# Performance work log

Hardware: AMD Instinct MI355X
Metric: run time of the kernel (lower is better)

## Reference

```python
import jax, jax.numpy as jnp
import numpy as np

TWN_THRESHOLD_FACTOR = 0.05
BN_EPS = 1e-5


def ternary_quantize(w):
    # threshold = 0.05 * max|w| (detached); q in {-1, 0, +1}
    t = TWN_THRESHOLD_FACTOR * jnp.max(jnp.abs(jax.lax.stop_gradient(w)))
    return (w > t).astype(w.dtype) - (w < -t).astype(w.dtype)


def conv2d(x, w, b):
    q = ternary_quantize(w)
    y = jax.lax.conv_general_dilated(x, q, (1, 1), 'VALID',
                                     dimension_numbers=('NCHW', 'OIHW', 'NCHW'))
    return y + b[None, :, None, None]


def linear(x, w, b):
    q = ternary_quantize(w)
    return x @ q.T + b


def bn_train(x, gamma, beta, axes):
    # training-mode batch norm (biased variance), matches torch BN in train()
    mean = jnp.mean(x, axis=axes, keepdims=True)
    var = jnp.var(x, axis=axes, keepdims=True)
    xhat = (x - mean) * jax.lax.rsqrt(var + BN_EPS)
    shape = [1] * x.ndim
    shape[1] = x.shape[1]
    return xhat * gamma.reshape(shape) + beta.reshape(shape)


def maxpool2(x):
    return jax.lax.reduce_window(x, -jnp.inf, jax.lax.max,
                                 (1, 1, 2, 2), (1, 1, 2, 2), 'VALID')


def setup_inputs() -> dict:
    key = jax.random.key(0)
    ks = jax.random.split(key, 8)
    B, Cin, H, W = 512, 1, 28, 28
    C1, C2, K = 64, 128, 5
    FLAT, F1, F2 = 4 * 4 * C2, 512, 10
    inp = {
        'x': jax.random.normal(ks[0], (B, Cin, H, W), jnp.float32),
        'conv1_w': jax.random.normal(ks[1], (C1, Cin, K, K), jnp.float32) * (1.0 / np.sqrt(Cin * K * K)),
        'conv1_b': jax.random.normal(ks[2], (C1,), jnp.float32) * 0.05,
        'bn1_g': jnp.ones((C1,), jnp.float32),
        'bn1_b': jnp.zeros((C1,), jnp.float32),
        'conv2_w': jax.random.normal(ks[3], (C2, C1, K, K), jnp.float32) * (1.0 / np.sqrt(C1 * K * K)),
        'conv2_b': jax.random.normal(ks[4], (C2,), jnp.float32) * 0.05,
        'bn2_g': jnp.ones((C2,), jnp.float32),
        'bn2_b': jnp.zeros((C2,), jnp.float32),
        'fc1_w': jax.random.normal(ks[5], (F1, FLAT), jnp.float32) * (1.0 / np.sqrt(FLAT)),
        'fc1_b': jax.random.normal(ks[6], (F1,), jnp.float32) * 0.05,
        'bn3_g': jnp.ones((F1,), jnp.float32),
        'bn3_b': jnp.zeros((F1,), jnp.float32),
        'fc2_w': jax.random.normal(ks[7], (F2, F1), jnp.float32) * (1.0 / np.sqrt(F1)),
        'fc2_b': jnp.zeros((F2,), jnp.float32),
    }
    return inp


def reference(x, conv1_w, conv1_b, bn1_g, bn1_b, conv2_w, conv2_b, bn2_g, bn2_b,
              fc1_w, fc1_b, bn3_g, bn3_b, fc2_w, fc2_b):
    h = jax.nn.relu(bn_train(conv2d(x, conv1_w, conv1_b), bn1_g, bn1_b, (0, 2, 3)))
    h = maxpool2(h)  # [B, 64, 12, 12]
    h = jax.nn.relu(bn_train(conv2d(h, conv2_w, conv2_b), bn2_g, bn2_b, (0, 2, 3)))
    h = maxpool2(h)  # [B, 128, 4, 4]
    h = h.reshape(h.shape[0], -1)  # [B, 2048]
    h = jax.nn.relu(bn_train(linear(h, fc1_w, fc1_b), bn3_g, bn3_b, (0,)))
    return linear(h, fc2_w, fc2_b)  # [B, 10]
```

## Files before the change

kernel.cpp:

```cpp
#include <hip/hip_runtime.h>
#include <stdint.h>

#define EPS 1e-5f

typedef short v8s __attribute__((ext_vector_type(8)));
typedef float v4f __attribute__((ext_vector_type(4)));

static const size_t W1F   = 4096;
static const size_t W2F   = 8192;
static const size_t WF2F  = 212992;
static const size_t A_F   = 262144;
static const size_t PMN2F = 4980736;
static const size_t B_F   = 19136512;
static const size_t WF1T  = B_F + 1048576;

__device__ inline unsigned short f2bf(float f) {
    unsigned u = __float_as_uint(f);
    return (unsigned short)((u + 0x7FFF + ((u >> 16) & 1)) >> 16);
}

__device__ __forceinline__ void stage16(const unsigned short* g, unsigned short* l) {
    __builtin_amdgcn_global_load_lds(
        (const __attribute__((address_space(1))) unsigned int*)g,
        (__attribute__((address_space(3))) unsigned int*)l, 16, 0, 0);
}

__global__ void k_zero(float* p, int n) {
    int i = blockIdx.x * blockDim.x + threadIdx.x;
    if (i < n) p[i] = 0.f;
}

__global__ void k_absmax4(const float* __restrict__ w0, int n0,
                          const float* __restrict__ w1, int n1,
                          const float* __restrict__ w2, int n2,
                          const float* __restrict__ w3, int n3,
                          float* outv) {
    int blk = blockIdx.x;
    const float* w; int n; unsigned* out; int nb; int bi;
    if (blk < 1)        { w = w0; n = n0; out = (unsigned*)(outv + 0); nb = 1;   bi = blk;      }
    else if (blk < 17)  { w = w1; n = n1; out = (unsigned*)(outv + 1); nb = 16;  bi = blk - 1;  }
    else if (blk < 209) { w = w2; n = n2; out = (unsigned*)(outv + 2); nb = 192; bi = blk - 17; }
    else                { w = w3; n = n3; out = (unsigned*)(outv + 3); nb = 1;   bi = blk - 209; }
    float m = 0.f;
    for (int i = bi * 256 + threadIdx.x; i < n; i += nb * 256)
        m = fmaxf(m, fabsf(w[i]));
    #pragma unroll
    for (int o = 32; o; o >>= 1) m = fmaxf(m, __shfl_down(m, o));
    if ((threadIdx.x & 63) == 0) atomicMax(out, __float_as_uint(m));
}

__global__ void k_quantE(const float* __restrict__ c1w, const float* __restrict__ c2w,
                         const float* __restrict__ f2w, const float* __restrict__ am,
                         float* __restrict__ w1t, unsigned short* __restrict__ w2u,
                         float* __restrict__ wf2) {
    int blk = blockIdx.x;
    if (blk < 1) {
        float t = 0.05f * am[0];
        for (int i = threadIdx.x; i < 1600; i += 256) {
            float v = c1w[i];
            float q = (float)((v > t) - (v < -t));
            int c = i / 25, k = i - c * 25;
            w1t[k * 64 + c] = q;
        }
    } else if (blk < 401) {
        float t = 0.05f * am[1];
        int base = (blk - 1) * 512;
        #pragma unroll
        for (int jj = 0; jj < 2; ++jj) {
            int i = base + jj * 256 + threadIdx.x;
            int j    = i & 7;
            int lane = (i >> 3) & 63;
            int mt   = (i >> 9) & 7;
            int ks   = (i >> 12) & 1;
            int p    = i >> 13;
            int c  = mt * 16 + (lane & 15);
            int ci = ks * 32 + (lane >> 4) * 8 + j;
            float v = c2w[c * 1600 + ci * 25 + p];
            w2u[i] = (v > t) ? (unsigned short)0x3F80
                             : ((v < -t) ? (unsigned short)0xBF80 : (unsigned short)0);
        }
    } else {
        float t = 0.05f * am[3];
        for (int i = threadIdx.x; i < 5120; i += 256) {
            float v = f2w[i];
            wf2[i] = (float)((v > t) - (v < -t));
        }
    }
}

__global__ __launch_bounds__(512) void k_conv1(const float* __restrict__ x,
                                               const float* __restrict__ w1t,
                                               unsigned* __restrict__ pmn1,
                                               float* __restrict__ sum,
                                               float* __restrict__ ssq) {
    __shared__ float xs[784];
    __shared__ float red[2][8][64];
    int b = blockIdx.x;
    const float4* xim = (const float4*)(x + (size_t)b * 784);
    for (int i = threadIdx.x; i < 196; i += 512) ((float4*)xs)[i] = xim[i];
    int c  = threadIdx.x & 63;
    int wv = threadIdx.x >> 6;
    float w[25];
    #pragma unroll
    for (int k = 0; k < 25; ++k) w[k] = w1t[k * 64 + c];
    __syncthreads();
    unsigned* ob = pmn1 + (size_t)b * 9216;
    float s = 0.f, s2 = 0.f;
    int ph = 0, pw = wv;
    for (int it = 0; it < 18; ++it) {
        const float* xp = xs + (ph * 2) * 28 + pw * 2;
        float win[36];
        #pragma unroll
        for (int i = 0; i < 6; ++i)
            #pragma unroll
            for (int j = 0; j < 3; ++j) {
                float2 t2 = *(const float2*)(xp + i * 28 + j * 2);
                win[i * 6 + j * 2] = t2.x; win[i * 6 + j * 2 + 1] = t2.y;
            }
        float v00 = 0.f, v01 = 0.f, v10 = 0.f, v11 = 0.f;
        #pragma unroll
        for (int i = 0; i < 5; ++i)
            #pragma unroll
            for (int j = 0; j < 5; ++j) {
                float wk = w[i * 5 + j];
                v00 = fmaf(win[i * 6 + j],           wk, v00);
                v01 = fmaf(win[i * 6 + j + 1],       wk, v01);
                v10 = fmaf(win[(i + 1) * 6 + j],     wk, v10);
                v11 = fmaf(win[(i + 1) * 6 + j + 1], wk, v11);
            }
        s  += v00 + v01 + v10 + v11;
        s2 += v00 * v00 + v01 * v01 + v10 * v10 + v11 * v11;
        float mx = fmaxf(fmaxf(v00, v01), fmaxf(v10, v11));
        float mn = fminf(fminf(v00, v01), fminf(v10, v11));
        ob[(ph * 12 + pw) * 64 + c] = ((unsigned)f2bf(mx) << 16) | (unsigned)f2bf(mn);
        pw += 8; if (pw >= 12) { pw -= 12; ++ph; }
    }
    red[0][wv][c] = s; red[1][wv][c] = s2;
    __syncthreads();
    if (threadIdx.x < 64) {
        float S = 0.f, S2 = 0.f;
        #pragma unroll
        for (int i = 0; i < 8; ++i) { S += red[0][i][threadIdx.x]; S2 += red[1][i][threadIdx.x]; }
        atomicAdd(&sum[threadIdx.x], S);
        atomicAdd(&ssq[threadIdx.x], S2);
    }
}

__global__ __launch_bounds__(256) void k_conv2(const unsigned* __restrict__ pmn1,
                                               const unsigned short* __restrict__ wfrag,
                                               const float* __restrict__ c1sum,
                                               const float* __restrict__ c1ssq,
                                               const float* __restrict__ g1,
                                               const float* __restrict__ b1,
                                               float* __restrict__ pmn,
                                               float* __restrict__ sum,
                                               float* __restrict__ ssq) {
    __shared__ unsigned short xs[144 * 76];
    __shared__ unsigned short wb[2][4096];
    __shared__ float reds[2][64], redq[2][64];
    int b     = blockIdx.x >> 1;
    int mhalf = blockIdx.x & 1;
    int tid  = threadIdx.x;
    int lane = tid & 63;
    int wave = tid >> 6;
    int nh = wave & 1, kp = wave >> 1;

    int ch0 = (tid & 15) * 4;
    float scv[4], shv[4];
    {
        const float invN = 1.f / 294912.f;
        #pragma unroll
        for (int j = 0; j < 4; ++j) {
            int ch = ch0 + j;
            float mean = c1sum[ch] * invN;
            float var  = c1ssq[ch] * invN - mean * mean;
            scv[j] = g1[ch] * rsqrtf(var + EPS);
            shv[j] = b1[ch] - mean * scv[j];
        }
    }
    const uint4* srcp = (const uint4*)(pmn1 + (size_t)b * 9216);
    for (int it = 0; it < 9; ++it) {
        int i = it * 256 + tid;
        int r = i >> 4;
        uint4 u4 = srcp[i];
        unsigned long long pack = 0;
        #pragma unroll
        for (int j = 0; j < 4; ++j) {
            unsigned u = (&u4.x)[j];
            float mx = __uint_as_float(u & 0xffff0000u);
            float mn = __uint_as_float(u << 16);
            float v = (scv[j] > 0.f) ? mx : mn;
            unsigned short o = f2bf(fmaxf(0.f, fmaf(v, scv[j], shv[j])));
            pack |= ((unsigned long long)o) << (16 * j);
        }
        *(unsigned long long*)(&xs[r * 76 + ch0]) = pack;
    }
    #pragma unroll
    for (int h = 0; h < 2; ++h) {
        int ksm = wave * 2 + h;
        int ks = ksm >> 2, mt = ksm & 3;
        const unsigned short* g = wfrag + (size_t)(ks * 8 + mhalf * 4 + mt) * 512 + lane * 8;
        stage16(g, &wb[0][ks * 2048 + mt * 512 + lane * 8]);
    }
    __syncthreads();

    int n = lane & 15, quad = lane >> 4;
    int ow = n & 7;
    int ohb0 = nh * 4 + (n >> 3);
    int col0 = kp * 32 + quad * 8;
    v4f acc[4][2];
    #pragma unroll
    for (int mm = 0; mm < 4; ++mm) { acc[mm][0] = (v4f){0,0,0,0}; acc[mm][1] = (v4f){0,0,0,0}; }
    for (int p = 0; p < 25; ++p) {
        int cur = p & 1;
        if (p < 24) {
            #pragma unroll
            for (int h = 0; h < 2; ++h) {
                int ksm = wave * 2 + h;
                int ks = ksm >> 2, mt = ksm & 3;
                const unsigned short* g = wfrag +
                    (size_t)(((p + 1) * 2 + ks) * 8 + mhalf * 4 + mt) * 512 + lane * 8;
                stage16(g, &wb[cur ^ 1][ks * 2048 + mt * 512 + lane * 8]);
            }
        }
        int kh = p / 5, kw = p - (p / 5) * 5;
        int col = (ow + kw) * 76 + col0;
        v8s bf0 = *(const v8s*)(&xs[(ohb0 + kh) * 912 + col]);
        v8s bf1 = *(const v8s*)(&xs[(ohb0 + 2 + kh) * 912 + col]);
        #pragma unroll
        for (int mm = 0; mm < 4; ++mm) {
            v8s af = *(const v8s*)(&wb[cur][kp * 2048 + mm * 512 + lane * 8]);
            acc[mm][0] = __builtin_amdgcn_mfma_f32_16x16x32_bf16(af, bf0, acc[mm][0], 0, 0, 0);
            acc[mm][1] = __builtin_amdgcn_mfma_f32_16x16x32_bf16(af, bf1, acc[mm][1], 0, 0, 0);
        }
        __syncthreads();
    }
    float* mbuf = (float*)xs;
    if (kp == 1) {
        float* d = mbuf + (nh * 64 + lane) * 36;
        #pragma unroll
        for (int mm = 0; mm < 4; ++mm) {
            *(v4f*)(d + mm * 8)     = acc[mm][0];
            *(v4f*)(d + mm * 8 + 4) = acc[mm][1];
        }
    }
    __syncthreads();
    if (kp == 0) {
        const float* s = mbuf + (nh * 64 + lane) * 36;
        #pragma unroll
        for (int mm = 0; mm < 4; ++mm) {
            acc[mm][0] += *(const v4f*)(s + mm * 8);
            acc[mm][1] += *(const v4f*)(s + mm * 8 + 4);
        }
        float* po = pmn + (size_t)b * 4096;
        #pragma unroll
        for (int mm = 0; mm < 4; ++mm) {
            int cl0 = mm * 16 + quad * 4;
            #pragma unroll
            for (int r = 0; r < 4; ++r) {
                int cl = cl0 + r;
                int c  = mhalf * 64 + cl;
                float sA = 0.f, s2A = 0.f;
                #pragma unroll
                for (int bf = 0; bf < 2; ++bf) {
                    float v = acc[mm][bf][r];
                    float pm = fmaxf(v, __shfl_xor(v, 1));
                    float pn = fminf(v, __shfl_xor(v, 1));
                    pm = fmaxf(pm, __shfl_xor(pm, 8));
                    pn = fminf(pn, __shfl_xor(pn, 8));
                    if (((n & 1) == 0) && (n < 8)) {
                        int psp = (nh * 2 + bf) * 4 + (n >> 1);
                        *(float2*)(&po[(c * 16 + psp) * 2]) = make_float2(pm, pn);
                    }
                    float s = v, s2 = v * v;
                    #pragma unroll
                    for (int m = 1; m < 16; m <<= 1) { s += __shfl_xor(s, m); s2 += __shfl_xor(s2, m); }
                    sA += s; s2A += s2;
                }
                if (n == 0) { reds[nh][cl] = sA; redq[nh][cl] = s2A; }
            }
        }
    }
    __syncthreads();
    if (tid < 64) {
        atomicAdd(&sum[mhalf * 64 + tid], reds[0][tid] + reds[1][tid]);
        atomicAdd(&ssq[mhalf * 64 + tid], redq[0][tid] + redq[1][tid]);
    }
}

__global__ void k_prep_fc1(const float* __restrict__ w, const float* __restrict__ am,
                           unsigned short* __restrict__ wf,
                           const float* __restrict__ pmn2, const float* __restrict__ c2sum,
                           const float* __restrict__ c2ssq, const float* __restrict__ g2,
                           const float* __restrict__ b2, unsigned short* __restrict__ xfrag) {
    if (blockIdx.x < 4096) {
        float t = 0.05f * am[2];
        int i = blockIdx.x * 256 + threadIdx.x;
        int f = i >> 11, k = i & 2047;
        float v = w[i];
        unsigned short q = (v > t) ? (unsigned short)0x3F80
                         : ((v < -t) ? (unsigned short)0xBF80 : (unsigned short)0);
        int ft = f >> 4, fm = f & 15;
        int ks = k >> 5, kr = k & 31;
        int lane = (kr >> 3) * 16 + fm;
        wf[((size_t)(ks * 32 + ft) * 64 + lane) * 8 + (kr & 7)] = q;
    } else {
        int i = (blockIdx.x - 4096) * 256 + threadIdx.x;
        int j    = i & 7;
        int lane = (i >> 3) & 63;
        int bt   = (i >> 9) & 31;
        int ks   = i >> 14;
        int b = bt * 16 + (lane & 15);
        int k = ks * 32 + (lane >> 4) * 8 + j;
        int c = k >> 4, psp = k & 15;
        float2 mm = *(const float2*)(&pmn2[((size_t)b * 2048 + c * 16 + psp) * 2]);
        float mean = c2sum[c] * (1.f / 32768.f);
        float var  = c2ssq[c] * (1.f / 32768.f) - mean * mean;
        float sc = g2[c] * rsqrtf(var + EPS);
        float sh = b2[c] - mean * sc;
        float v = (sc > 0.f) ? mm.x : mm.y;
        xfrag[i] = f2bf(fmaxf(0.f, fmaf(v, sc, sh)));
    }
}

__global__ __launch_bounds__(256) void k_fc1(const unsigned short* __restrict__ xfrag,
                                             const unsigned short* __restrict__ wfrag,
                                             float* __restrict__ out,
                                             float* __restrict__ sum,
                                             float* __restrict__ ssq) {
    int lane = threadIdx.x & 63;
    int wave = threadIdx.x >> 6;
    int ft = (blockIdx.x & 7) * 4 + wave;
    int bT = blockIdx.x >> 3;
    v4f acc = (v4f){0.f, 0.f, 0.f, 0.f};
    for (int ks = 0; ks < 64; ++ks) {
        v8s bfrag = *(const v8s*)(xfrag + ((size_t)(ks * 32 + bT) * 64 + lane) * 8);
        v8s afrag = *(const v8s*)(wfrag + ((size_t)(ks * 32 + ft) * 64 + lane) * 8);
        acc = __builtin_amdgcn_mfma_f32_16x16x32_bf16(afrag, bfrag, acc, 0, 0, 0);
    }
    int bb = bT * 16 + (lane & 15);
    int quad = lane >> 4;
    int f0 = ft * 16 + quad * 4;
    *(float4*)(&out[(size_t)bb * 512 + f0]) =
        make_float4(acc[0], acc[1], acc[2], acc[3]);
    #pragma unroll
    for (int r = 0; r < 4; ++r) {
        float s = acc[r], s2 = s * s;
        #pragma unroll
        for (int m = 1; m < 16; m <<= 1) { s += __shfl_xor(s, m); s2 += __shfl_xor(s2, m); }
        if ((lane & 15) == 0) { atomicAdd(&sum[f0 + r], s); atomicAdd(&ssq[f0 + r], s2); }
    }
}

__global__ __launch_bounds__(256) void k_fc2(const float* __restrict__ x,
                                             const float* __restrict__ w,
                                             const float* __restrict__ bias,
                                             const float* __restrict__ fsum,
                                             const float* __restrict__ fssq,
                                             const float* __restrict__ g3,
                                             const float* __restrict__ b3,
                                             float* __restrict__ out) {
    int lane = threadIdx.x & 63;
    int b = blockIdx.x * 4 + (threadIdx.x >> 6);
    float xa[8], sm[8], sq[8], ga[8], ba[8];
    {
        const float4* p;
        p = (const float4*)(x + (size_t)b * 512 + lane * 8);
        *(float4*)xa = p[0]; *(float4*)(xa + 4) = p[1];
        p = (const float4*)(fsum + lane * 8);
        *(float4*)sm = p[0]; *(float4*)(sm + 4) = p[1];
        p = (const float4*)(fssq + lane * 8);
        *(float4*)sq = p[0]; *(float4*)(sq + 4) = p[1];
        p = (const float4*)(g3 + lane * 8);
        *(float4*)ga = p[0]; *(float4*)(ga + 4) = p[1];
        p = (const float4*)(b3 + lane * 8);
        *(float4*)ba = p[0]; *(float4*)(ba + 4) = p[1];
    }
    float h[8];
    #pragma unroll
    for (int e = 0; e < 8; ++e) {
        float mean = sm[e] * (1.f / 512.f);
        float var  = sq[e] * (1.f / 512.f) - mean * mean;
        float sc = ga[e] * rsqrtf(var + EPS);
        float sh = ba[e] - mean * sc;
        h[e] = fmaxf(0.f, fmaf(xa[e], sc, sh));
    }
    #pragma unroll
    for (int j = 0; j < 10; ++j) {
        const float4* wp = (const float4*)(w + j * 512 + lane * 8);
        float4 w0 = wp[0], w1 = wp[1];
        float p = h[0] * w0.x + h[1] * w0.y + h[2] * w0.z + h[3] * w0.w
                + h[4] * w1.x + h[5] * w1.y + h[6] * w1.z + h[7] * w1.w;
        #pragma unroll
        for (int o = 32; o; o >>= 1) p += __shfl_down(p, o);
        if (lane == 0) out[b * 10 + j] = p + bias[j];
    }
}

extern "C" void kernel_launch(void* const* d_in, const int* in_sizes, int n_in,
                              void* d_out, int out_size, void* d_ws, size_t ws_size,
                              hipStream_t stream) {
    const float* x       = (const float*)d_in[0];
    const float* conv1_w = (const float*)d_in[1];
    const float* bn1_g   = (const float*)d_in[3];
    const float* bn1_b   = (const float*)d_in[4];
    const float* conv2_w = (const float*)d_in[5];
    const float* bn2_g   = (const float*)d_in[7];
    const float* bn2_b   = (const float*)d_in[8];
    const float* fc1_w   = (const float*)d_in[9];
    const float* bn3_g   = (const float*)d_in[11];
    const float* bn3_b   = (const float*)d_in[12];
    const float* fc2_w   = (const float*)d_in[13];
    const float* fc2_b   = (const float*)d_in[14];

    float* wsf = (float*)d_ws;

    float* c1_sum = wsf + 16,   * c1_ssq = wsf + 80;
    float* c2_sum = wsf + 272,  * c2_ssq = wsf + 400;
    float* f_sum  = wsf + 1808, * f_ssq  = wsf + 2320;

    float* w1t = wsf + W1F;
    unsigned short* w2u = (unsigned short*)(wsf + W2F);
    float* wf2 = wsf + WF2F;
    unsigned short* wf1 = (unsigned short*)(wsf + WF1T);
    unsigned* PMN1 = (unsigned*)(wsf + A_F);
    float* PMN2 = wsf + PMN2F;
    float* A    = wsf + A_F;
    unsigned short* xfrag = (unsigned short*)(wsf + B_F);

    k_zero<<<16, 256, 0, stream>>>(wsf, 4096);

    k_absmax4<<<210, 256, 0, stream>>>(conv1_w, 1600, conv2_w, 204800,
                                       fc1_w, 1048576, fc2_w, 5120, wsf);

    k_quantE<<<402, 256, 0, stream>>>(conv1_w, conv2_w, fc2_w, wsf, w1t, w2u, wf2);

    k_conv1<<<512, 512, 0, stream>>>(x, w1t, PMN1, c1_sum, c1_ssq);

    k_conv2<<<1024, 256, 0, stream>>>(PMN1, w2u, c1_sum, c1_ssq, bn1_g, bn1_b,
                                      PMN2, c2_sum, c2_ssq);

    k_prep_fc1<<<8192, 256, 0, stream>>>(fc1_w, wsf, wf1, PMN2, c2_sum, c2_ssq,
                                         bn2_g, bn2_b, xfrag);

    k_fc1<<<256, 256, 0, stream>>>(xfrag, wf1, A, f_sum, f_ssq);

    k_fc2<<<128, 256, 0, stream>>>(A, wf2, fc2_b, f_sum, f_ssq, bn3_g, bn3_b,
                                   (float*)d_out);
}
```

Baseline: 201.3 us.

## Fuse zeroing, absmax and weight quantization into fewer launches; streamline conv2 loop

Merges the zero, absmax and quantize kernels into two launches. Absmax now writes per-block partial maxima instead of using atomics, and conv1 quantizes its own weights inline. fc1 weight quantization moves into the conv1 launch as extra blocks, so it runs concurrently instead of in a later prep kernel. The conv2 main loop is restructured with a lambda that uses incremental pointers and ping-pong buffers to remove per-iteration index arithmetic. Every consumer block re-reduces up to 192 partial maxima serially, which adds some redundant work.

Measured after the change: 210.7 us. +4.7%, slower.

```diff
diff --git a/kernel.cpp b/kernel.cpp
--- a/kernel.cpp
+++ b/kernel.cpp
@@ -6,7 +6,6 @@
 typedef short v8s __attribute__((ext_vector_type(8)));
 typedef float v4f __attribute__((ext_vector_type(4)));
 
-static const size_t W1F   = 4096;
 static const size_t W2F   = 8192;
 static const size_t WF2F  = 212992;
 static const size_t A_F   = 262144;
@@ -14,6 +13,11 @@
 static const size_t B_F   = 19136512;
 static const size_t WF1T  = B_F + 1048576;
 
+#define P_C1 1024
+#define P_F2 1025
+#define P_C2 1040
+#define P_F1 1240
+
 __device__ inline unsigned short f2bf(float f) {
     unsigned u = __float_as_uint(f);
     return (unsigned short)((u + 0x7FFF + ((u >> 16) & 1)) >> 16);
@@ -25,84 +29,106 @@
         (__attribute__((address_space(3))) unsigned int*)l, 16, 0, 0);
 }
 
-__global__ void k_zero(float* p, int n) {
-    int i = blockIdx.x * blockDim.x + threadIdx.x;
-    if (i < n) p[i] = 0.f;
-}
-
-__global__ void k_absmax4(const float* __restrict__ w0, int n0,
-                          const float* __restrict__ w1, int n1,
-                          const float* __restrict__ w2, int n2,
-                          const float* __restrict__ w3, int n3,
-                          float* outv) {
+__global__ void k_absz(const float* __restrict__ c1w, const float* __restrict__ c2w,
+                       const float* __restrict__ f1w, const float* __restrict__ f2w,
+                       float* __restrict__ wsf) {
+    __shared__ float sm4[4];
     int blk = blockIdx.x;
-    const float* w; int n; unsigned* out; int nb; int bi;
-    if (blk < 1)        { w = w0; n = n0; out = (unsigned*)(outv + 0); nb = 1;   bi = blk;      }
-    else if (blk < 17)  { w = w1; n = n1; out = (unsigned*)(outv + 1); nb = 16;  bi = blk - 1;  }
-    else if (blk < 209) { w = w2; n = n2; out = (unsigned*)(outv + 2); nb = 192; bi = blk - 17; }
-    else                { w = w3; n = n3; out = (unsigned*)(outv + 3); nb = 1;   bi = blk - 209; }
+    if (blk >= 384) {
+        if (blk < 386) {
+            int i = (blk - 384) * 256 + threadIdx.x + 16;
+            if (i < 528) wsf[i] = 0.f;
+        } else {
+            int i = (blk - 386) * 256 + threadIdx.x + 1808;
+            if (i < 2832) wsf[i] = 0.f;
+        }
+        return;
+    }
+    const float* w; int n; int nb; int bi; float* out;
+    if (blk == 0)       { w = c1w; n = 1600;    nb = 1;   bi = 0;         out = wsf + P_C1; }
+    else if (blk == 1)  { w = f2w; n = 5120;    nb = 1;   bi = 0;         out = wsf + P_F2; }
+    else if (blk < 194) { w = c2w; n = 204800;  nb = 192; bi = blk - 2;   out = wsf + P_C2 + bi; }
+    else                { w = f1w; n = 1048576; nb = 190; bi = blk - 194; out = wsf + P_F1 + bi; }
     float m = 0.f;
     for (int i = bi * 256 + threadIdx.x; i < n; i += nb * 256)
         m = fmaxf(m, fabsf(w[i]));
     #pragma unroll
     for (int o = 32; o; o >>= 1) m = fmaxf(m, __shfl_down(m, o));
-    if ((threadIdx.x & 63) == 0) atomicMax(out, __float_as_uint(m));
-}
-
-__global__ void k_quantE(const float* __restrict__ c1w, const float* __restrict__ c2w,
-                         const float* __restrict__ f2w, const float* __restrict__ am,
-                         float* __restrict__ w1t, unsigned short* __restrict__ w2u,
-                         float* __restrict__ wf2) {
+    if ((threadIdx.x & 63) == 0) sm4[threadIdx.x >> 6] = m;
+    __syncthreads();
+    if (threadIdx.x == 0)
+        *out = fmaxf(fmaxf(sm4[0], sm4[1]), fmaxf(sm4[2], sm4[3]));
+}
+
+__global__ __launch_bounds__(512) void k_mid(const float* __restrict__ x,
+                                             const float* __restrict__ c1w,
+                                             const float* __restrict__ c2w,
+                                             const float* __restrict__ f1w,
+                                             const float* __restrict__ f2w,
+                                             float* __restrict__ wsf,
+                                             unsigned* __restrict__ pmn1,
+                                             unsigned short* __restrict__ w2u,
+                                             unsigned short* __restrict__ wf1,
+                                             float* __restrict__ wf2) {
     int blk = blockIdx.x;
-    if (blk < 1) {
-        float t = 0.05f * am[0];
-        for (int i = threadIdx.x; i < 1600; i += 256) {
-            float v = c1w[i];
-            float q = (float)((v > t) - (v < -t));
-            int c = i / 25, k = i - c * 25;
-            w1t[k * 64 + c] = q;
-        }
-    } else if (blk < 401) {
-        float t = 0.05f * am[1];
-        int base = (blk - 1) * 512;
-        #pragma unroll
-        for (int jj = 0; jj < 2; ++jj) {
-            int i = base + jj * 256 + threadIdx.x;
-            int j    = i & 7;
-            int lane = (i >> 3) & 63;
-            int mt   = (i >> 9) & 7;
-            int ks   = (i >> 12) & 1;
-            int p    = i >> 13;
-            int c  = mt * 16 + (lane & 15);
-            int ci = ks * 32 + (lane >> 4) * 8 + j;
-            float v = c2w[c * 1600 + ci * 25 + p];
-            w2u[i] = (v > t) ? (unsigned short)0x3F80
-                             : ((v < -t) ? (unsigned short)0xBF80 : (unsigned short)0);
-        }
-    } else {
-        float t = 0.05f * am[3];
-        for (int i = threadIdx.x; i < 5120; i += 256) {
-            float v = f2w[i];
-            wf2[i] = (float)((v > t) - (v < -t));
-        }
-    }
-}
-
-__global__ __launch_bounds__(512) void k_conv1(const float* __restrict__ x,
-                                               const float* __restrict__ w1t,
-                                               unsigned* __restrict__ pmn1,
-                                               float* __restrict__ sum,
-                                               float* __restrict__ ssq) {
+    int tid = threadIdx.x;
+    if (blk >= 512) {
+        if (blk < 612) {
+            float m = 0.f;
+            for (int i = 0; i < 192; ++i) m = fmaxf(m, wsf[P_C2 + i]);
+            float t = 0.05f * m;
+            for (int i = (blk - 512) * 512 + tid; i < 204800; i += 100 * 512) {
+                int j    = i & 7;
+                int lane = (i >> 3) & 63;
+                int mt   = (i >> 9) & 7;
+                int ks   = (i >> 12) & 1;
+                int p    = i >> 13;
+                int c  = mt * 16 + (lane & 15);
+                int ci = ks * 32 + (lane >> 4) * 8 + j;
+                float v = c2w[c * 1600 + ci * 25 + p];
+                w2u[i] = (v > t) ? (unsigned short)0x3F80
+                                 : ((v < -t) ? (unsigned short)0xBF80 : (unsigned short)0);
+            }
+        } else if (blk < 868) {
+            float m = 0.f;
+            for (int i = 0; i < 190; ++i) m = fmaxf(m, wsf[P_F1 + i]);
+            float t = 0.05f * m;
+            for (int i = (blk - 612) * 512 + tid; i < 1048576; i += 256 * 512) {
+                float v = f1w[i];
+                unsigned short q = (v > t) ? (unsigned short)0x3F80
+                                 : ((v < -t) ? (unsigned short)0xBF80 : (unsigned short)0);
+                int f = i >> 11, k = i & 2047;
+                int ft = f >> 4, fm = f & 15;
+                int ks = k >> 5, kr = k & 31;
+                int lane = (kr >> 3) * 16 + fm;
+                wf1[((size_t)(ks * 32 + ft) * 64 + lane) * 8 + (kr & 7)] = q;
+            }
+        } else {
+            float t = 0.05f * wsf[P_F2];
+            for (int i = tid; i < 5120; i += 512) {
+                float v = f2w[i];
+                wf2[i] = (float)((v > t) - (v < -t));
+            }
+        }
+        return;
+    }
     __shared__ float xs[784];
     __shared__ float red[2][8][64];
-    int b = blockIdx.x;
+    int b = blk;
     const float4* xim = (const float4*)(x + (size_t)b * 784);
-    for (int i = threadIdx.x; i < 196; i += 512) ((float4*)xs)[i] = xim[i];
-    int c  = threadIdx.x & 63;
-    int wv = threadIdx.x >> 6;
+    for (int i = tid; i < 196; i += 512) ((float4*)xs)[i] = xim[i];
+    int c  = tid & 63;
+    int wv = tid >> 6;
     float w[25];
-    #pragma unroll
-    for (int k = 0; k < 25; ++k) w[k] = w1t[k * 64 + c];
+    {
+        float t = 0.05f * wsf[P_C1];
+        const float* src = c1w + c * 25;
+        #pragma unroll
+        for (int k = 0; k < 25; ++k) {
+            float v = src[k];
+            w[k] = (float)((v > t) - (v < -t));
+        }
+    }
     __syncthreads();
     unsigned* ob = pmn1 + (size_t)b * 9216;
     float s = 0.f, s2 = 0.f;
@@ -137,12 +163,12 @@
     }
     red[0][wv][c] = s; red[1][wv][c] = s2;
     __syncthreads();
-    if (threadIdx.x < 64) {
+    if (tid < 64) {
         float S = 0.f, S2 = 0.f;
         #pragma unroll
-        for (int i = 0; i < 8; ++i) { S += red[0][i][threadIdx.x]; S2 += red[1][i][threadIdx.x]; }
-        atomicAdd(&sum[threadIdx.x], S);
-        atomicAdd(&ssq[threadIdx.x], S2);
+        for (int i = 0; i < 8; ++i) { S += red[0][i][tid]; S2 += red[1][i][tid]; }
+        atomicAdd(&wsf[16 + tid], S);
+        atomicAdd(&wsf[80 + tid], S2);
     }
 }
 
@@ -195,46 +221,54 @@
         }
         *(unsigned long long*)(&xs[r * 76 + ch0]) = pack;
     }
-    #pragma unroll
-    for (int h = 0; h < 2; ++h) {
-        int ksm = wave * 2 + h;
-        int ks = ksm >> 2, mt = ksm & 3;
-        const unsigned short* g = wfrag + (size_t)(ks * 8 + mhalf * 4 + mt) * 512 + lane * 8;
-        stage16(g, &wb[0][ks * 2048 + mt * 512 + lane * 8]);
-    }
+    int ksm0 = wave * 2, ksm1 = wave * 2 + 1;
+    int ks0 = ksm0 >> 2, mt0 = ksm0 & 3;
+    int ks1 = ksm1 >> 2, mt1 = ksm1 & 3;
+    const unsigned short* g0 = wfrag + (size_t)(ks0 * 8 + mhalf * 4 + mt0) * 512 + lane * 8;
+    const unsigned short* g1p = wfrag + (size_t)(ks1 * 8 + mhalf * 4 + mt1) * 512 + lane * 8;
+    const int l0 = ks0 * 2048 + mt0 * 512 + lane * 8;
+    const int l1 = ks1 * 2048 + mt1 * 512 + lane * 8;
+    stage16(g0,  &wb[0][l0]);
+    stage16(g1p, &wb[0][l1]);
+    g0 += 8192; g1p += 8192;
     __syncthreads();
 
     int n = lane & 15, quad = lane >> 4;
     int ow = n & 7;
     int ohb0 = nh * 4 + (n >> 3);
     int col0 = kp * 32 + quad * 8;
+    const int lb = kp * 2048 + lane * 8;
+    int a0 = ohb0 * 912 + ow * 76 + col0;
+    int kw = 0;
     v4f acc[4][2];
     #pragma unroll
     for (int mm = 0; mm < 4; ++mm) { acc[mm][0] = (v4f){0,0,0,0}; acc[mm][1] = (v4f){0,0,0,0}; }
-    for (int p = 0; p < 25; ++p) {
-        int cur = p & 1;
-        if (p < 24) {
-            #pragma unroll
-            for (int h = 0; h < 2; ++h) {
-                int ksm = wave * 2 + h;
-                int ks = ksm >> 2, mt = ksm & 3;
-                const unsigned short* g = wfrag +
-                    (size_t)(((p + 1) * 2 + ks) * 8 + mhalf * 4 + mt) * 512 + lane * 8;
-                stage16(g, &wb[cur ^ 1][ks * 2048 + mt * 512 + lane * 8]);
-            }
-        }
-        int kh = p / 5, kw = p - (p / 5) * 5;
-        int col = (ow + kw) * 76 + col0;
-        v8s bf0 = *(const v8s*)(&xs[(ohb0 + kh) * 912 + col]);
-        v8s bf1 = *(const v8s*)(&xs[(ohb0 + 2 + kh) * 912 + col]);
+
+    auto step = [&](const unsigned short* wbR, unsigned short* wbW, bool st) {
+        if (st) {
+            stage16(g0,  wbW + l0);
+            stage16(g1p, wbW + l1);
+            g0 += 8192; g1p += 8192;
+        }
+        v8s bf0 = *(const v8s*)(xs + a0);
+        v8s bf1 = *(const v8s*)(xs + a0 + 1824);
         #pragma unroll
         for (int mm = 0; mm < 4; ++mm) {
-            v8s af = *(const v8s*)(&wb[cur][kp * 2048 + mm * 512 + lane * 8]);
+            v8s af = *(const v8s*)(wbR + lb + mm * 512);
             acc[mm][0] = __builtin_amdgcn_mfma_f32_16x16x32_bf16(af, bf0, acc[mm][0], 0, 0, 0);
             acc[mm][1] = __builtin_amdgcn_mfma_f32_16x16x32_bf16(af, bf1, acc[mm][1], 0, 0, 0);
         }
         __syncthreads();
-    }
+        a0 += (kw == 4) ? 608 : 76;
+        kw = (kw == 4) ? 0 : kw + 1;
+    };
+    #pragma unroll 1
+    for (int pp = 0; pp < 12; ++pp) {
+        step(&wb[0][0], &wb[1][0], true);
+        step(&wb[1][0], &wb[0][0], true);
+    }
+    step(&wb[0][0], &wb[1][0], false);
+
     float* mbuf = (float*)xs;
     if (kp == 1) {
         float* d = mbuf + (nh * 64 + lane) * 36;
@@ -259,7 +293,7 @@
             #pragma unroll
             for (int r = 0; r < 4; ++r) {
                 int cl = cl0 + r;
-                int c  = mhalf * 64 + cl;
+                int cc = mhalf * 64 + cl;
                 float sA = 0.f, s2A = 0.f;
                 #pragma unroll
                 for (int bf = 0; bf < 2; ++bf) {
@@ -270,7 +304,7 @@
                     pn = fminf(pn, __shfl_xor(pn, 8));
                     if (((n & 1) == 0) && (n < 8)) {
                         int psp = (nh * 2 + bf) * 4 + (n >> 1);
-                        *(float2*)(&po[(c * 16 + psp) * 2]) = make_float2(pm, pn);
+                        *(float2*)(&po[(cc * 16 + psp) * 2]) = make_float2(pm, pn);
                     }
                     float s = v, s2 = v * v;
                     #pragma unroll
@@ -288,39 +322,24 @@
     }
 }
 
-__global__ void k_prep_fc1(const float* __restrict__ w, const float* __restrict__ am,
-                           unsigned short* __restrict__ wf,
-                           const float* __restrict__ pmn2, const float* __restrict__ c2sum,
-                           const float* __restrict__ c2ssq, const float* __restrict__ g2,
-                           const float* __restrict__ b2, unsigned short* __restrict__ xfrag) {
-    if (blockIdx.x < 4096) {
-        float t = 0.05f * am[2];
-        int i = blockIdx.x * 256 + threadIdx.x;
-        int f = i >> 11, k = i & 2047;
-        float v = w[i];
-        unsigned short q = (v > t) ? (unsigned short)0x3F80
-                         : ((v < -t) ? (unsigned short)0xBF80 : (unsigned short)0);
-        int ft = f >> 4, fm = f & 15;
-        int ks = k >> 5, kr = k & 31;
-        int lane = (kr >> 3) * 16 + fm;
-        wf[((size_t)(ks * 32 + ft) * 64 + lane) * 8 + (kr & 7)] = q;
-    } else {
-        int i = (blockIdx.x - 4096) * 256 + threadIdx.x;
-        int j    = i & 7;
-        int lane = (i >> 3) & 63;
-        int bt   = (i >> 9) & 31;
-        int ks   = i >> 14;
-        int b = bt * 16 + (lane & 15);
-        int k = ks * 32 + (lane >> 4) * 8 + j;
-        int c = k >> 4, psp = k & 15;
-        float2 mm = *(const float2*)(&pmn2[((size_t)b * 2048 + c * 16 + psp) * 2]);
-        float mean = c2sum[c] * (1.f / 32768.f);
-        float var  = c2ssq[c] * (1.f / 32768.f) - mean * mean;
-        float sc = g2[c] * rsqrtf(var + EPS);
-        float sh = b2[c] - mean * sc;
-        float v = (sc > 0.f) ? mm.x : mm.y;
-        xfrag[i] = f2bf(fmaxf(0.f, fmaf(v, sc, sh)));
-    }
+__global__ void k_bnpool2(const float* __restrict__ pmn2, const float* __restrict__ c2sum,
+                          const float* __restrict__ c2ssq, const float* __restrict__ g2,
+                          const float* __restrict__ b2, unsigned short* __restrict__ xfrag) {
+    int i = blockIdx.x * 256 + threadIdx.x;
+    int j    = i & 7;
+    int lane = (i >> 3) & 63;
+    int bt   = (i >> 9) & 31;
+    int ks   = i >> 14;
+    int b = bt * 16 + (lane & 15);
+    int k = ks * 32 + (lane >> 4) * 8 + j;
+    int c = k >> 4, psp = k & 15;
+    float2 mm = *(const float2*)(&pmn2[((size_t)b * 2048 + c * 16 + psp) * 2]);
+    float mean = c2sum[c] * (1.f / 32768.f);
+    float var  = c2ssq[c] * (1.f / 32768.f) - mean * mean;
+    float sc = g2[c] * rsqrtf(var + EPS);
+    float sh = b2[c] - mean * sc;
+    float v = (sc > 0.f) ? mm.x : mm.y;
+    xfrag[i] = f2bf(fmaxf(0.f, fmaf(v, sc, sh)));
 }
 
 __global__ __launch_bounds__(256) void k_fc1(const unsigned short* __restrict__ xfrag,
@@ -419,7 +438,6 @@
     float* c2_sum = wsf + 272,  * c2_ssq = wsf + 400;
     float* f_sum  = wsf + 1808, * f_ssq  = wsf + 2320;
 
-    float* w1t = wsf + W1F;
     unsigned short* w2u = (unsigned short*)(wsf + W2F);
     float* wf2 = wsf + WF2F;
     unsigned short* wf1 = (unsigned short*)(wsf + WF1T);
@@ -428,20 +446,15 @@
     float* A    = wsf + A_F;
     unsigned short* xfrag = (unsigned short*)(wsf + B_F);
 
-    k_zero<<<16, 256, 0, stream>>>(wsf, 4096);
-
-    k_absmax4<<<210, 256, 0, stream>>>(conv1_w, 1600, conv2_w, 204800,
-                                       fc1_w, 1048576, fc2_w, 5120, wsf);
-
-    k_quantE<<<402, 256, 0, stream>>>(conv1_w, conv2_w, fc2_w, wsf, w1t, w2u, wf2);
-
-    k_conv1<<<512, 512, 0, stream>>>(x, w1t, PMN1, c1_sum, c1_ssq);
+    k_absz<<<390, 256, 0, stream>>>(conv1_w, conv2_w, fc1_w, fc2_w, wsf);
+
+    k_mid<<<869, 512, 0, stream>>>(x, conv1_w, conv2_w, fc1_w, fc2_w, wsf,
+                                   PMN1, w2u, wf1, wf2);
 
     k_conv2<<<1024, 256, 0, stream>>>(PMN1, w2u, c1_sum, c1_ssq, bn1_g, bn1_b,
                                       PMN2, c2_sum, c2_ssq);
 
-    k_prep_fc1<<<8192, 256, 0, stream>>>(fc1_w, wsf, wf1, PMN2, c2_sum, c2_ssq,
-                                         bn2_g, bn2_b, xfrag);
+    k_bnpool2<<<4096, 256, 0, stream>>>(PMN2, c2_sum, c2_ssq, bn2_g, bn2_b, xfrag);
 
     k_fc1<<<256, 256, 0, stream>>>(xfrag, wf1, A, f_sum, f_ssq);
 
```
